# Performance work log

Hardware: AMD Instinct MI355X
Metric: run time of the kernel (lower is better)

The kernel has to match this reference:

```python
import jax, jax.numpy as jnp
import numpy as np

# KWConv2d config: in=256, out=256, k=3, s=1, p=1, groups=1, bias=False
# warehouse: 32 spatial cells of shape [64, 64, 3, 3]; num_fourier_basis=0; temp_value=0
B, CIN, H, W_ = 32, 256, 56, 56
OUT = 256
NUM_CELLS, CO, CI, KH, KW = 32, 64, 64, 3, 3
HIDDEN = 16                 # max(int(256 * 0.0625), 16)
GO, GI, GS = OUT // CO, CIN // CI, 1
M = GO * GI * GS            # num_local_mixture = 16
P = NUM_CELLS + 1           # kw_planes_per_mixture = 33
KWP = P * M                 # kw_planes = 528


def setup_inputs() -> dict:
    key = jax.random.key(0)
    ks = jax.random.split(key, 4)
    s = 0.02
    return {
        "x": jax.random.normal(ks[0], (B, CIN, H, W_), jnp.float32),
        "cells": jax.random.normal(ks[1], (NUM_CELLS, CO, CI, KH, KW), jnp.float32) * s,
        "fc1_w": jax.random.normal(ks[2], (HIDDEN, CIN), jnp.float32) * s,
        "fc1_b": jnp.zeros((HIDDEN,), jnp.float32),
        "ln_g": jnp.ones((HIDDEN,), jnp.float32),
        "ln_b": jnp.zeros((HIDDEN,), jnp.float32),
        "sp_w": jax.random.normal(ks[3], (KWP, HIDDEN), jnp.float32) * s,
        "sp_b": jnp.zeros((KWP,), jnp.float32),
    }


def _attention(x, fc1_w, fc1_b, ln_g, ln_b, sp_w, sp_b):
    # AdaptiveAvgPool1d(1) over flattened spatial dims == global mean
    pooled = x.mean(axis=(2, 3))                      # [B, CIN]
    h = pooled @ fc1_w.T + fc1_b                      # [B, HIDDEN]
    mu = h.mean(-1, keepdims=True)
    var = ((h - mu) ** 2).mean(-1, keepdims=True)
    h = (h - mu) * jax.lax.rsqrt(var + 1e-5) * ln_g + ln_b
    h = jax.nn.relu(h)
    a = h @ sp_w.T + sp_b                             # spatial_head -> [B, KWP]
    a = a.reshape(-1, P)                              # [B*M, P]
    a = a / (jnp.abs(a).sum(axis=1, keepdims=True) + 0.001)  # L1 normalize per mixture
    # temp_value = 0 -> attention unchanged; drop last (zero) column
    return a[:, :-1]                                  # [B*M, NUM_CELLS]


def reference(x, cells, fc1_w, fc1_b, ln_g, ln_b, sp_w, sp_b):
    att = _attention(x, fc1_w, fc1_b, ln_g, ln_b, sp_w, sp_b)  # [B*M, NUM_CELLS]
    w = cells.reshape(NUM_CELLS, -1)                  # [NUM_CELLS, CO*CI*KH*KW]
    agg = att @ w                                     # [B*M, CO*CI*KH*KW]
    agg = agg.reshape(B, GS, GO, GI, CO, CI, KH, KW)
    agg = agg.transpose(0, 2, 4, 3, 5, 1, 6, 7)       # torch permute (0,2,4,3,5,1,6,7)
    agg = agg.reshape(B * OUT, CIN, KH, KW)           # per-sample kernels (groups=1)
    # grouped-conv trick: fold batch into channels, groups = B
    xr = x.reshape(1, B * CIN, H, W_)
    out = jax.lax.conv_general_dilated(
        xr, agg, window_strides=(1, 1), padding=((1, 1), (1, 1)),
        dimension_numbers=("NCHW", "OIHW", "NCHW"), feature_group_count=B)
    return out.reshape(B, OUT, H, W_)
```

## Files before the change

### kernel.cpp

```cpp
#include <hip/hip_runtime.h>
#include <stdint.h>

typedef unsigned short ush;
typedef __bf16   bf16x8 __attribute__((ext_vector_type(8)));
typedef float    f32x4  __attribute__((ext_vector_type(4)));
typedef uint32_t u32x4  __attribute__((ext_vector_type(4)));

union U16B { u32x4 u; bf16x8 b; };
union P8   { ush us[8]; u32x4 v; };

template<int V> struct ICx { static constexpr int value = V; };

__device__ __forceinline__ ush f2bf(float f) {
    union { float f; uint32_t u; } v; v.f = f;
    uint32_t r = v.u + 0x7FFFu + ((v.u >> 16) & 1u);
    return (ush)(r >> 16);
}

__device__ __forceinline__ void gl_lds16(const ush* g, ush* l) {
    __builtin_amdgcn_global_load_lds(
        (const __attribute__((address_space(1))) uint32_t*)g,
        (__attribute__((address_space(3))) uint32_t*)l, 16, 0, 0);
}

#define HWPX  3136
#define POOL_OFF   58720256UL
#define ATT_OFF    58753024UL
#define WAGG_OFF   58818560UL

__global__ void k_transpose(const float* __restrict__ x, ush* __restrict__ xT,
                            float* __restrict__ pooled) {
    __shared__ float tile[64][65];
    int blk = blockIdx.x;
    int b   = blk / 196;
    int rem = blk % 196;
    int icg = rem / 49;
    int pxg = rem % 49;
    int t = threadIdx.x;

    {
        int icl  = t >> 2, part = t & 3;
        const float* src = x + (size_t)(b * 256 + icg * 64 + icl) * HWPX + pxg * 64 + part * 16;
        #pragma unroll
        for (int k = 0; k < 4; ++k) {
            f32x4 v = *(const f32x4*)(src + k * 4);
            tile[icl][part * 16 + k * 4 + 0] = v[0];
            tile[icl][part * 16 + k * 4 + 1] = v[1];
            tile[icl][part * 16 + k * 4 + 2] = v[2];
            tile[icl][part * 16 + k * 4 + 3] = v[3];
        }
    }

    if (t < 32) {
        int r = (pxg * 64 + 55) / 56 + (t >> 4);
        if (r < 56 && r * 56 <= pxg * 64 + 63) {
            int icg32 = icg * 2 + ((t >> 3) & 1);
            int colp  = ((t >> 2) & 1) ? 57 : 0;
            int chunk = t & 3;
            u32x4 z = (u32x4)(0u);
            *(u32x4*)(xT + (((size_t)(b * 8 + icg32) * 56 + r) * 64 + colp) * 32 + chunk * 8) = z;
        }
    }
    __syncthreads();

    if (t < 64) {
        float s = 0.f;
        #pragma unroll 8
        for (int p = 0; p < 64; ++p) s += tile[t][p];
        atomicAdd(pooled + b * 256 + icg * 64 + t, s);
    }

    {
        int pxl = t >> 2, icq = t & 3;
        int px  = pxg * 64 + pxl;
        int row = px / 56;
        int col = px - row * 56;
        int p   = col + 1;
        int xorp = (p >> 1) & 3;
        int icg32   = icg * 2 + (icq >> 1);
        int subbase = (icq & 1) * 2;
        P8 lo, hi;
        #pragma unroll
        for (int m = 0; m < 8; ++m) {
            lo.us[m] = f2bf(tile[icq * 16 + m][pxl]);
            hi.us[m] = f2bf(tile[icq * 16 + 8 + m][pxl]);
        }
        size_t base = (((size_t)(b * 8 + icg32) * 56 + row) * 64 + p) * 32;
        *(u32x4*)(xT + base + (size_t)((subbase ^ xorp) * 8))       = lo.v;
        *(u32x4*)(xT + base + (size_t)(((subbase + 1) ^ xorp) * 8)) = hi.v;
    }
}

__global__ void k_attn(const float* __restrict__ pooled,
                       const float* __restrict__ fc1_w, const float* __restrict__ fc1_b,
                       const float* __restrict__ ln_g,  const float* __restrict__ ln_b,
                       const float* __restrict__ sp_w,  const float* __restrict__ sp_b,
                       float* __restrict__ att) {
    __shared__ float hs[32][16];
    int t = threadIdx.x;
    {
        int b = t >> 4, j = t & 15;
        float acc = 0.f;
        for (int c = 0; c < 256; ++c) acc += pooled[b * 256 + c] * fc1_w[j * 256 + c];
        hs[b][j] = fc1_b[j] + acc * (1.0f / 3136.0f);
    }
    __syncthreads();
    if (t < 32) {
        float mu = 0.f;
        #pragma unroll
        for (int j = 0; j < 16; ++j) mu += hs[t][j];
        mu *= (1.0f / 16.0f);
        float var = 0.f;
        #pragma unroll
        for (int j = 0; j < 16; ++j) { float d = hs[t][j] - mu; var += d * d; }
        var *= (1.0f / 16.0f);
        float inv = rsqrtf(var + 1e-5f);
        #pragma unroll
        for (int j = 0; j < 16; ++j) {
            float v = (hs[t][j] - mu) * inv * ln_g[j] + ln_b[j];
            hs[t][j] = fmaxf(v, 0.f);
        }
    }
    __syncthreads();
    {
        int b = t >> 4, m = t & 15;
        float a[33];
        #pragma unroll 1
        for (int i = 0; i < 33; ++i) {
            int p = m * 33 + i;
            float acc = sp_b[p];
            #pragma unroll
            for (int j = 0; j < 16; ++j) acc += hs[b][j] * sp_w[p * 16 + j];
            a[i] = acc;
        }
        float s = 0.f;
        #pragma unroll
        for (int i = 0; i < 33; ++i) s += fabsf(a[i]);
        float inv = 1.0f / (s + 0.001f);
        #pragma unroll
        for (int c = 0; c < 32; ++c) att[(b * 16 + m) * 32 + c] = a[c] * inv;
    }
}

__global__ void k_agg(const float* __restrict__ cells, const float* __restrict__ att,
                      ush* __restrict__ wagg) {
    __shared__ float at[512];
    int blk = blockIdx.x;
    int b = blk >> 6, co = blk & 63;
    int t = threadIdx.x;
    for (int i = t; i < 512; i += 256) at[i] = att[b * 512 + i];
    __syncthreads();
    int ci = t & 63, gi = t >> 6;
    float acc[4][9];
    #pragma unroll
    for (int g = 0; g < 4; ++g)
        #pragma unroll
        for (int k = 0; k < 9; ++k) acc[g][k] = 0.f;
    for (int c = 0; c < 32; ++c) {
        float a0 = at[(0 + gi) * 32 + c];
        float a1 = at[(4 + gi) * 32 + c];
        float a2 = at[(8 + gi) * 32 + c];
        float a3 = at[(12 + gi) * 32 + c];
        const float* cp = cells + (size_t)c * 36864 + co * 576 + ci * 9;
        #pragma unroll
        for (int k = 0; k < 9; ++k) {
            float cv = cp[k];
            acc[0][k] += a0 * cv; acc[1][k] += a1 * cv;
            acc[2][k] += a2 * cv; acc[3][k] += a3 * cv;
        }
    }
    #pragma unroll
    for (int g = 0; g < 4; ++g)
        #pragma unroll
        for (int k = 0; k < 9; ++k)
            wagg[((size_t)(b * 9 + k) * 256 + g * 64 + co) * 256 + gi * 64 + ci] = f2bf(acc[g][k]);
}

__global__ __launch_bounds__(256, 2) void k_conv(const ush* __restrict__ xT,
                                                 const ush* __restrict__ wagg,
                                                 float* __restrict__ out) {
    __shared__ __align__(16) ush xs[2][12288];
    __shared__ __align__(16) ush wsh[16384];

    int tid = threadIdx.x;
    int wg  = blockIdx.x;
    int xcd = wg & 7;
    int kk  = wg >> 3;
    int gq  = kk / 14;
    int sp  = kk - gq * 14;
    int g   = gq * 8 + xcd;
    int b   = g >> 2, octile = g & 3;
    int row0 = sp * 4, oc0 = octile * 64;

    int lane = tid & 63, w = tid >> 6;
    int wn = w & 1, ocH = w >> 1;
    int l15 = lane & 15, s4 = lane >> 4;

    {
        u32x4 z = (u32x4)(0u);
        #pragma unroll
        for (int i = 0; i < 12; ++i) ((u32x4*)xs)[tid + i * 256] = z;
    }

    int prow[7], pq[7];
    #pragma unroll
    for (int j = 0; j < 7; ++j) {
        int px = wn * 112 + j * 16 + l15;
        prow[j] = px / 56;
        pq[j]   = px - prow[j] * 56;
    }

    unsigned vmask = 0;
    #pragma unroll
    for (int k = 0; k < 6; ++k) {
        int grow = row0 - 1 + k;
        if (grow >= 0 && grow < 56) vmask |= 1u << k;
    }

    const ush* wgl  = wagg + (size_t)b * 9 * 65536 + (size_t)(oc0 + (tid >> 2)) * 256 + (tid & 3) * 8;
    ush*       wdst = wsh + ((size_t)(tid & 3) * 64 + (tid >> 2)) * 8;
    const ush* wrd  = wsh + ((size_t)s4 * 64 + ocH * 32 + l15) * 8;
    const ush* w8gl = wagg + (size_t)(b * 9 + 8) * 65536 + (size_t)(oc0 + ocH * 32 + l15) * 256 + s4 * 8;
    const ush* xb = xT + (size_t)b * 8 * 56 * 2048 + (size_t)tid * 8;

    f32x4 acc[2][7];
    #pragma unroll
    for (int mi = 0; mi < 2; ++mi)
        #pragma unroll
        for (int j = 0; j < 7; ++j) acc[mi][j] = (f32x4)(0.f);

    __syncthreads();

    {
        U16B wpre[8];
        #pragma unroll
        for (int k = 0; k < 8; ++k) wpre[k].u = *(const u32x4*)(wgl + (size_t)k * 65536);
        #pragma unroll
        for (int k = 0; k < 6; ++k)
            if (vmask & (1u << k))
                gl_lds16(xb + (size_t)(row0 - 1 + k) * 2048, &xs[0][0] + k * 2048 + w * 512);
        __syncthreads();
        #pragma unroll
        for (int k = 0; k < 8; ++k) *(u32x4*)(wdst + k * 2048) = wpre[k].u;
        __syncthreads();
    }

    auto chunk_body = [&](auto parc, int cc) {
        constexpr int PAR = decltype(parc)::value;
        U16B wf8[2];
        wf8[0].u = *(const u32x4*)(w8gl + (size_t)cc * 32);
        wf8[1].u = *(const u32x4*)(w8gl + (size_t)cc * 32 + 4096);
        U16B wpre[8];
        bool pre = cc < 7;
        if (pre) {
            const ush* wgc = wgl + (size_t)(cc + 1) * 32;
            #pragma unroll
            for (int k = 0; k < 8; ++k) wpre[k].u = *(const u32x4*)(wgc + (size_t)k * 65536);
            ush* xo = &xs[0][0] + (PAR ^ 1) * 12288;
            #pragma unroll
            for (int k = 0; k < 6; ++k)
                if (vmask & (1u << k))
                    gl_lds16(xb + (size_t)((cc + 1) * 56 + row0 - 1 + k) * 2048,
                             xo + k * 2048 + w * 512);
        }
        const ush* xsb = &xs[0][0] + PAR * 12288;
        #pragma unroll
        for (int tap = 0; tap < 8; ++tap) {
            const int dy = tap / 3, dx = tap % 3;
            U16B wf[2];
            wf[0].u = *(const u32x4*)(wrd + tap * 2048);
            wf[1].u = *(const u32x4*)(wrd + tap * 2048 + 128);
            U16B bx[7];
            #pragma unroll
            for (int j = 0; j < 7; ++j) {
                int q    = pq[j] + dx;
                int slot = s4 ^ ((q >> 1) & 3);
                bx[j].u = *(const u32x4*)(xsb + ((prow[j] + dy) * 64 + q) * 32 + slot * 8);
            }
            __builtin_amdgcn_s_setprio(1);
            #pragma unroll
            for (int j = 0; j < 7; ++j) {
                acc[0][j] = __builtin_amdgcn_mfma_f32_16x16x32_bf16(bx[j].b, wf[0].b, acc[0][j], 0, 0, 0);
                acc[1][j] = __builtin_amdgcn_mfma_f32_16x16x32_bf16(bx[j].b, wf[1].b, acc[1][j], 0, 0, 0);
            }
            __builtin_amdgcn_s_setprio(0);
        }
        {
            U16B bx[7];
            #pragma unroll
            for (int j = 0; j < 7; ++j) {
                int q    = pq[j] + 2;
                int slot = s4 ^ ((q >> 1) & 3);
                bx[j].u = *(const u32x4*)(xsb + ((prow[j] + 2) * 64 + q) * 32 + slot * 8);
            }
            __builtin_amdgcn_s_setprio(1);
            #pragma unroll
            for (int j = 0; j < 7; ++j) {
                acc[0][j] = __builtin_amdgcn_mfma_f32_16x16x32_bf16(bx[j].b, wf8[0].b, acc[0][j], 0, 0, 0);
                acc[1][j] = __builtin_amdgcn_mfma_f32_16x16x32_bf16(bx[j].b, wf8[1].b, acc[1][j], 0, 0, 0);
            }
            __builtin_amdgcn_s_setprio(0);
        }
        __syncthreads();
        if (pre) {
            #pragma unroll
            for (int k = 0; k < 8; ++k) *(u32x4*)(wdst + k * 2048) = wpre[k].u;
            __syncthreads();
        }
    };

    for (int c2 = 0; c2 < 8; c2 += 2) {
        chunk_body(ICx<0>{}, c2);
        chunk_body(ICx<1>{}, c2 + 1);
    }

    int pxbase = row0 * 56 + wn * 112 + s4 * 4;
    #pragma unroll
    for (int mi = 0; mi < 2; ++mi) {
        int oc = oc0 + ocH * 32 + mi * 16 + l15;
        float* o = out + (size_t)(b * 256 + oc) * HWPX + pxbase;
        #pragma unroll
        for (int j = 0; j < 7; ++j)
            *(f32x4*)(o + j * 16) = acc[mi][j];
    }
}

extern "C" void kernel_launch(void* const* d_in, const int* in_sizes, int n_in,
                              void* d_out, int out_size, void* d_ws, size_t ws_size,
                              hipStream_t stream) {
    const float* x     = (const float*)d_in[0];
    const float* cells = (const float*)d_in[1];
    const float* fc1_w = (const float*)d_in[2];
    const float* fc1_b = (const float*)d_in[3];
    const float* ln_g  = (const float*)d_in[4];
    const float* ln_b  = (const float*)d_in[5];
    const float* sp_w  = (const float*)d_in[6];
    const float* sp_b  = (const float*)d_in[7];
    float* out = (float*)d_out;

    char* ws = (char*)d_ws;
    ush*   xT     = (ush*)ws;
    float* pooled = (float*)(ws + POOL_OFF);
    float* att    = (float*)(ws + ATT_OFF);
    ush*   wagg   = (ush*)(ws + WAGG_OFF);

    hipMemsetAsync(pooled, 0, 32768, stream);
    k_transpose<<<6272, 256, 0, stream>>>(x, xT, pooled);
    k_attn<<<1, 512, 0, stream>>>(pooled, fc1_w, fc1_b, ln_g, ln_b, sp_w, sp_b, att);
    k_agg<<<2048, 256, 0, stream>>>(cells, att, wagg);
    k_conv<<<1792, 256, 0, stream>>>(xT, wagg, out);
}
```

Before: 240.6 us.

## Pre-tile aggregated weights and stream them to LDS via async double-buffered loads

The weight aggregation kernel now writes per-sample weights in a chunked, LDS-ready layout ordered by (sample, channel chunk, octile, tap, slot, oc, ic). The conv kernel loads these with global_load_lds directly into two half-buffers of weight taps, replacing the register staging and LDS store. Each chunk is split into two phases with explicit waitcnt and barrier calls, so the loads for the second half and the next chunk overlap with MFMA work. This removes register pressure and a barrier-plus-store step. In exchange the kernel depends on hand-counted vmcnt values that must match the number of outstanding loads.

```diff
diff --git a/kernel.cpp b/kernel.cpp
--- a/kernel.cpp
+++ b/kernel.cpp
@@ -169,18 +169,23 @@
             acc[2][k] += a2 * cv; acc[3][k] += a3 * cv;
         }
     }
+    int ic  = gi * 64 + ci;
+    int cc  = ic >> 5;
+    int s   = (ic >> 3) & 3;
+    int icw = ic & 7;
     #pragma unroll
     for (int g = 0; g < 4; ++g)
         #pragma unroll
         for (int k = 0; k < 9; ++k)
-            wagg[((size_t)(b * 9 + k) * 256 + g * 64 + co) * 256 + gi * 64 + ci] = f2bf(acc[g][k]);
+            wagg[((size_t)(b * 32 + cc * 4 + g) * 9 + k) * 2048 + s * 512 + co * 8 + icw]
+                = f2bf(acc[g][k]);
 }
 
 __global__ __launch_bounds__(256, 2) void k_conv(const ush* __restrict__ xT,
                                                  const ush* __restrict__ wagg,
                                                  float* __restrict__ out) {
     __shared__ __align__(16) ush xs[2][12288];
-    __shared__ __align__(16) ush wsh[16384];
+    __shared__ __align__(16) ush wsh[2][8192];
 
     int tid = threadIdx.x;
     int wg  = blockIdx.x;
@@ -216,11 +221,11 @@
         int grow = row0 - 1 + k;
         if (grow >= 0 && grow < 56) vmask |= 1u << k;
     }
-
-    const ush* wgl  = wagg + (size_t)b * 9 * 65536 + (size_t)(oc0 + (tid >> 2)) * 256 + (tid & 3) * 8;
-    ush*       wdst = wsh + ((size_t)(tid & 3) * 64 + (tid >> 2)) * 8;
-    const ush* wrd  = wsh + ((size_t)s4 * 64 + ocH * 32 + l15) * 8;
-    const ush* w8gl = wagg + (size_t)(b * 9 + 8) * 65536 + (size_t)(oc0 + ocH * 32 + l15) * 256 + s4 * 8;
+    const bool full6 = (vmask == 0x3Fu);
+
+    const ush* wc0 = wagg + ((size_t)b * 32 + octile) * 9 * 2048;
+    const int  woff = s4 * 512 + (ocH * 32 + l15) * 8;
+    const ush* w8gl = wc0 + 8 * 2048 + woff;
     const ush* xb = xT + (size_t)b * 8 * 56 * 2048 + (size_t)tid * 8;
 
     f32x4 acc[2][7];
@@ -231,60 +236,78 @@
 
     __syncthreads();
 
-    {
-        U16B wpre[8];
-        #pragma unroll
-        for (int k = 0; k < 8; ++k) wpre[k].u = *(const u32x4*)(wgl + (size_t)k * 65536);
-        #pragma unroll
-        for (int k = 0; k < 6; ++k)
-            if (vmask & (1u << k))
-                gl_lds16(xb + (size_t)(row0 - 1 + k) * 2048, &xs[0][0] + k * 2048 + w * 512);
-        __syncthreads();
-        #pragma unroll
-        for (int k = 0; k < 8; ++k) *(u32x4*)(wdst + k * 2048) = wpre[k].u;
-        __syncthreads();
-    }
+    #pragma unroll
+    for (int k = 0; k < 4; ++k)
+        gl_lds16(wc0 + (w * 4 + k) * 512 + lane * 8, &wsh[0][(w * 4 + k) * 512]);
+    #pragma unroll
+    for (int k = 0; k < 6; ++k)
+        if (vmask & (1u << k))
+            gl_lds16(xb + (size_t)(row0 - 1 + k) * 2048, &xs[0][k * 2048 + w * 512]);
+    __syncthreads();
+
+    auto do_tap = [&](const ush* xsb, const ush* wfp, int dy, int dx) {
+        U16B wf[2];
+        wf[0].u = *(const u32x4*)(wfp);
+        wf[1].u = *(const u32x4*)(wfp + 128);
+        U16B bx[7];
+        #pragma unroll
+        for (int j = 0; j < 7; ++j) {
+            int q    = pq[j] + dx;
+            int slot = s4 ^ ((q >> 1) & 3);
+            bx[j].u = *(const u32x4*)(xsb + ((prow[j] + dy) * 64 + q) * 32 + slot * 8);
+        }
+        __builtin_amdgcn_s_setprio(1);
+        #pragma unroll
+        for (int j = 0; j < 7; ++j) {
+            acc[0][j] = __builtin_amdgcn_mfma_f32_16x16x32_bf16(bx[j].b, wf[0].b, acc[0][j], 0, 0, 0);
+            acc[1][j] = __builtin_amdgcn_mfma_f32_16x16x32_bf16(bx[j].b, wf[1].b, acc[1][j], 0, 0, 0);
+        }
+        __builtin_amdgcn_s_setprio(0);
+    };
 
     auto chunk_body = [&](auto parc, int cc) {
         constexpr int PAR = decltype(parc)::value;
+        const ush* xsb = &xs[PAR][0];
+        const ush* wck = wc0 + (size_t)cc * 73728;
+
         U16B wf8[2];
-        wf8[0].u = *(const u32x4*)(w8gl + (size_t)cc * 32);
-        wf8[1].u = *(const u32x4*)(w8gl + (size_t)cc * 32 + 4096);
-        U16B wpre[8];
-        bool pre = cc < 7;
-        if (pre) {
-            const ush* wgc = wgl + (size_t)(cc + 1) * 32;
-            #pragma unroll
-            for (int k = 0; k < 8; ++k) wpre[k].u = *(const u32x4*)(wgc + (size_t)k * 65536);
-            ush* xo = &xs[0][0] + (PAR ^ 1) * 12288;
+        wf8[0].u = *(const u32x4*)(w8gl + (size_t)cc * 73728);
+        wf8[1].u = *(const u32x4*)(w8gl + (size_t)cc * 73728 + 128);
+        #pragma unroll
+        for (int k = 0; k < 4; ++k)
+            gl_lds16(wck + 8192 + (w * 4 + k) * 512 + lane * 8,
+                     &wsh[1][(w * 4 + k) * 512]);
+        __builtin_amdgcn_sched_barrier(0);
+        if (cc < 7) {
             #pragma unroll
             for (int k = 0; k < 6; ++k)
                 if (vmask & (1u << k))
                     gl_lds16(xb + (size_t)((cc + 1) * 56 + row0 - 1 + k) * 2048,
-                             xo + k * 2048 + w * 512);
-        }
-        const ush* xsb = &xs[0][0] + PAR * 12288;
-        #pragma unroll
-        for (int tap = 0; tap < 8; ++tap) {
-            const int dy = tap / 3, dx = tap % 3;
-            U16B wf[2];
-            wf[0].u = *(const u32x4*)(wrd + tap * 2048);
-            wf[1].u = *(const u32x4*)(wrd + tap * 2048 + 128);
-            U16B bx[7];
-            #pragma unroll
-            for (int j = 0; j < 7; ++j) {
-                int q    = pq[j] + dx;
-                int slot = s4 ^ ((q >> 1) & 3);
-                bx[j].u = *(const u32x4*)(xsb + ((prow[j] + dy) * 64 + q) * 32 + slot * 8);
-            }
-            __builtin_amdgcn_s_setprio(1);
-            #pragma unroll
-            for (int j = 0; j < 7; ++j) {
-                acc[0][j] = __builtin_amdgcn_mfma_f32_16x16x32_bf16(bx[j].b, wf[0].b, acc[0][j], 0, 0, 0);
-                acc[1][j] = __builtin_amdgcn_mfma_f32_16x16x32_bf16(bx[j].b, wf[1].b, acc[1][j], 0, 0, 0);
-            }
-            __builtin_amdgcn_s_setprio(0);
-        }
+                             &xs[PAR ^ 1][k * 2048 + w * 512]);
+        }
+        do_tap(xsb, &wsh[0][0 * 2048 + woff], 0, 0);
+        do_tap(xsb, &wsh[0][1 * 2048 + woff], 0, 1);
+        do_tap(xsb, &wsh[0][2 * 2048 + woff], 0, 2);
+        do_tap(xsb, &wsh[0][3 * 2048 + woff], 1, 0);
+        asm volatile("s_waitcnt lgkmcnt(0)" ::: "memory");
+        if (cc < 7) {
+            if (full6) asm volatile("s_waitcnt vmcnt(6)" ::: "memory");
+            else       asm volatile("s_waitcnt vmcnt(5)" ::: "memory");
+        } else {
+            asm volatile("s_waitcnt vmcnt(0)" ::: "memory");
+        }
+        __builtin_amdgcn_s_barrier();
+
+        if (cc < 7) {
+            #pragma unroll
+            for (int k = 0; k < 4; ++k)
+                gl_lds16(wck + 73728 + (w * 4 + k) * 512 + lane * 8,
+                         &wsh[0][(w * 4 + k) * 512]);
+        }
+        do_tap(xsb, &wsh[1][0 * 2048 + woff], 1, 1);
+        do_tap(xsb, &wsh[1][1 * 2048 + woff], 1, 2);
+        do_tap(xsb, &wsh[1][2 * 2048 + woff], 2, 0);
+        do_tap(xsb, &wsh[1][3 * 2048 + woff], 2, 1);
         {
             U16B bx[7];
             #pragma unroll
@@ -301,12 +324,9 @@
             }
             __builtin_amdgcn_s_setprio(0);
         }
-        __syncthreads();
-        if (pre) {
-            #pragma unroll
-            for (int k = 0; k < 8; ++k) *(u32x4*)(wdst + k * 2048) = wpre[k].u;
-            __syncthreads();
-        }
+        asm volatile("s_waitcnt lgkmcnt(0)" ::: "memory");
+        asm volatile("s_waitcnt vmcnt(0)" ::: "memory");
+        __builtin_amdgcn_s_barrier();
     };
 
     for (int c2 = 0; c2 < 8; c2 += 2) {
```

New measurement: 237.4 us. No clear change (-1.3%).
